# Optimization experiments

Measured on AMD Instinct MI355X. Metric: run time of the kernel, lower is better.

The kernel has to match this reference:

```python
import math
import jax, jax.numpy as jnp
import numpy as np
from jax import lax

B, N, F = 16, 1024, 35  # graphs, nodes, one-hot label width
HID = 2000

def leaky(x):
    return jnp.where(x >= 0, x, 0.01 * x)

def spp(x, levels, mode):
    # x: [C,H,W]; faithful port of spatial_pyramid_pool.spp (per-level pool,
    # flatten, zero-pad to p*p). Pool params are static Python ints.
    C, H, W = x.shape
    outs = []
    for p in range(1, levels + 1):
        kh, kw = math.ceil(H / p), math.ceil(W / p)
        ph, pw = kh * p - H, kw * p - W
        if ph * 2 > kh:
            ph = kh // 2
        if pw * 2 > kw:
            pw = kw // 2
        pad = [(0, 0), (ph, ph), (pw, pw)]
        if mode == 'max':
            r = lax.reduce_window(x, -jnp.inf, lax.max, (1, kh, kw), (1, kh, kw), pad)
        else:  # avg, count_include_pad=True (torch default)
            r = lax.reduce_window(x, 0.0, lax.add, (1, kh, kw), (1, kh, kw), pad) / (kh * kw)
        flat = r.reshape(C, -1)
        flat = jnp.pad(flat, ((0, 0), (0, p * p - flat.shape[1])))
        outs.append(flat)
    return jnp.concatenate(outs, axis=1)  # [C, sum_p p^2]

def wlc(x, masks, K):
    # Vectorized weisfeiler_lehman_conv_switch.WLC.
    # x: [N,F]; masks: [4,N,N] one-hot of edge type s in {1..4}; K: [C,T,4,F].
    # Each convo step (snapshot semantics via cal_list.clone()):
    #   x_new[i] = x[i] + sum_j [s_ij==k+1] * x[j] * K[t,k]
    def one_channel(Kc):  # Kc: [T,4,F]
        def step(xc, Kt):
            return xc + jnp.einsum('kij,jf,kf->if', masks, xc, Kt), None
        xc, _ = lax.scan(step, x, Kc)
        return xc
    return jax.vmap(one_channel)(K)  # [C,N,F]

def conv2d(x, w, b):
    y = lax.conv_general_dilated(x, w, (1, 1), 'VALID',
                                 dimension_numbers=('NCHW', 'OIHW', 'NCHW'))
    return y + b[None, :, None, None]

def setup_inputs() -> dict:
    key = jax.random.key(0)
    ks = jax.random.split(key, 16)
    lin_in = 4 * sum((i + 1) ** 2 for i in range(10)) + 5 * sum((i + 1) ** 2 for i in range(3))  # 1610
    f32 = jnp.float32
    return {
        'labelsList': jax.random.normal(ks[0], (B, N, F), f32),
        'ligand_structure': jax.random.randint(ks[1], (B, N, N), 0, 5).astype(f32),
        'K1': jax.random.normal(ks[2], (2, 2, 4, F), f32) * 0.05,
        'K2': jax.random.normal(ks[3], (2, 2, 4, F), f32) * 0.05,
        'cw1': jax.random.normal(ks[4], (2, 1, 3, 3), f32) * 0.2,
        'cb1': jnp.zeros((2,), f32),
        'cw2': jax.random.normal(ks[5], (5, 2, 3, 3), f32) * 0.1,
        'cb2': jnp.zeros((5,), f32),
        'W1': jax.random.normal(ks[6], (HID, lin_in), f32) * 0.02,
        'b1': jnp.zeros((HID,), f32),
        'W2': jax.random.normal(ks[7], (HID, HID), f32) * 0.02,
        'b2': jnp.zeros((HID,), f32),
        'W3': jax.random.normal(ks[8], (HID, HID), f32) * 0.02,
        'b3': jnp.zeros((HID,), f32),
        'W4': jax.random.normal(ks[9], (HID, HID), f32) * 0.02,
        'b4': jnp.zeros((HID,), f32),
        'W5': jax.random.normal(ks[10], (2, HID), f32) * 0.02,
        'b5': jnp.zeros((2,), f32),
    }

def reference(labelsList, ligand_structure, K1, K2, cw1, cb1, cw2, cb2,
              W1, b1, W2, b2, W3, b3, W4, b4, W5, b5):
    def per_sample(x, s):  # x: [N,F], s: [N,N]
        masks = (s[None] == jnp.arange(1.0, 5.0, dtype=s.dtype)[:, None, None]).astype(x.dtype)
        c1 = leaky(wlc(x, masks, K1))                       # [2,N,F]
        c2 = jax.vmap(lambda xc: wlc(xc, masks, K2))(c1)    # [2,2,N,F], cat order matches torch
        c2 = c2.reshape(4, N, F)
        feat = spp(leaky(c2), 10, 'max').reshape(-1)        # [1540]
        z = s[None, None]                                   # [1,1,N,N]
        z = leaky(conv2d(z, cw1, cb1))
        z = leaky(conv2d(z, cw2, cb2))                      # [1,5,N-4,N-4]
        stru = spp(z[0], 3, 'avg').reshape(-1)              # [70]
        return jnp.concatenate([feat, stru])                # [1610]

    h = jax.vmap(per_sample)(labelsList, ligand_structure)  # [B,1610]
    # fc_model (dropout = identity in eval)
    h = leaky(h @ W1.T + b1)
    h = leaky(h @ W2.T + b2)
    h = leaky(h @ W3.T + b3)
    h = leaky(h @ W4.T + b4)
    return h @ W5.T + b5                                    # [B,2]
```

## Files before the change

kernel.cpp:

```cpp
#include <hip/hip_runtime.h>
#include <stdint.h>

#define NN 1024
#define FF 35
#define LIN_IN 1610
#define NB 16

typedef short short8 __attribute__((ext_vector_type(8)));
typedef float f32x4 __attribute__((ext_vector_type(4)));
typedef float f32x2 __attribute__((ext_vector_type(2)));

__device__ __forceinline__ float leakyf(float x) { return fmaxf(x, 0.01f * x); }
__device__ __forceinline__ uint16_t to_bf16(float v) {
    return (uint16_t)((__float_as_uint(v) + 0x8000u) >> 16);
}
__device__ __forceinline__ f32x2 sp2(float s) { return (f32x2){s, s}; }
__device__ __forceinline__ f32x2 leaky2(f32x2 v) {
    f32x2 r;
    r.x = fmaxf(v.x, 0.01f * v.x);
    r.y = fmaxf(v.y, 0.01f * v.y);
    return r;
}
__device__ __forceinline__ uint32_t mapf(float x) {
    uint32_t u = __float_as_uint(x);
    return (u & 0x80000000u) ? ~u : (u | 0x80000000u);
}
__device__ __forceinline__ float unmapf(uint32_t u) {
    return (u & 0x80000000u) ? __uint_as_float(u & 0x7FFFFFFFu) : __uint_as_float(~u);
}

__global__ __launch_bounds__(256)
void codes_kernel(const float* __restrict__ s, uint8_t* __restrict__ codes, int n4) {
    int i = blockIdx.x * 256 + threadIdx.x;
    for (; i < n4; i += gridDim.x * 256) {
        float4 v = ((const float4*)s)[i];
        uchar4 c;
        c.x = (uint8_t)v.x; c.y = (uint8_t)v.y; c.z = (uint8_t)v.z; c.w = (uint8_t)v.w;
        ((uchar4*)codes)[i] = c;
    }
}

__global__ __launch_bounds__(256)
void labels_to_xt(const float* __restrict__ labels, uint16_t* __restrict__ XT0,
                  float* __restrict__ XR0)
{
    __shared__ float buf[256 * FF];
    const int s = blockIdx.x;
    const int i0 = blockIdx.y * 256;
    const float* src = labels + ((size_t)s * NN + i0) * FF;
    for (int t = threadIdx.x; t < 256 * FF; t += 256) buf[t] = src[t];
    __syncthreads();
    for (int f = 0; f < 48; ++f) {
        const int ii = threadIdx.x;
        float v = (f < FF) ? buf[ii * FF + f] : 0.f;
        size_t o = ((size_t)s * 48 + f) * 1024 + i0 + ii;
        XR0[o] = v;
        XT0[o] = to_bf16(v);
    }
}

__device__ __forceinline__ short8 expand_onehot(uint2 cd, uint32_t dupK) {
    union { uint32_t u[4]; short8 v; } r;
#pragma unroll
    for (int h = 0; h < 2; ++h) {
        uint32_t d = h ? cd.y : cd.x;
        uint32_t y = d ^ dupK;
        uint32_t m = (~(((y & 0x7F7F7F7Fu) + 0x7F7F7F7Fu) | y)) & 0x80808080u;
        uint32_t m2 = m >> 7;
        r.u[h * 2 + 0] = ((m2 & 0xFFu) | ((m2 & 0xFF00u) << 8)) * 0x3F80u;
        r.u[h * 2 + 1] = (((m2 >> 16) & 0xFFu) | ((m2 >> 8) & 0xFF0000u)) * 0x3F80u;
    }
    return r.v;
}

__device__ __forceinline__
void wlc_body(int mt, int nt, int s,
              const uint16_t* __restrict__ XT_in, const float* __restrict__ XR_in,
              uint16_t* __restrict__ XT_out, float* __restrict__ XR_out,
              const uint8_t* __restrict__ codes, const float* __restrict__ Kg,
              int t, int shift, int nch_in, int nch_out, int do_leaky)
{
    const int tid   = threadIdx.x;
    const int wid   = tid >> 6;
    const int lane  = tid & 63;
    const int chout = nt;
    const int inch  = chout >> shift;
    const int kch   = chout & 1;
    const int i0    = mt * 64 + wid * 16;

    const uint8_t* cbase = codes + ((size_t)s << 20)
        + (size_t)(i0 + (lane & 15)) * 1024 + ((lane >> 4) << 3);
    const uint16_t* bbase = XT_in + (((size_t)s * nch_in + inch) * 48 + (lane & 15)) * 1024
        + ((lane >> 4) << 3);

    f32x4 acc[4][3];
#pragma unroll
    for (int k = 0; k < 4; ++k)
#pragma unroll
        for (int nf = 0; nf < 3; ++nf) acc[k][nf] = (f32x4){0.f, 0.f, 0.f, 0.f};

#pragma unroll 2
    for (int jt = 0; jt < 16; ++jt) {
        const int j0 = jt * 64;
        const uint2 cd0 = *(const uint2*)(cbase + j0);
        const uint2 cd1 = *(const uint2*)(cbase + j0 + 32);

        short8 bfr[3][2];
#pragma unroll
        for (int nf = 0; nf < 3; ++nf)
#pragma unroll
            for (int kk = 0; kk < 2; ++kk)
                bfr[nf][kk] = *(const short8*)(bbase + (size_t)nf * 16 * 1024 + j0 + kk * 32);

#pragma unroll
        for (int k = 0; k < 4; ++k) {
            const uint32_t dupK = 0x01010101u * (k + 1);
#pragma unroll
            for (int kk = 0; kk < 2; ++kk) {
                short8 af = expand_onehot(kk ? cd1 : cd0, dupK);
#pragma unroll
                for (int nf = 0; nf < 3; ++nf)
                    acc[k][nf] = __builtin_amdgcn_mfma_f32_16x16x32_bf16(
                        af, bfr[nf][kk], acc[k][nf], 0, 0, 0);
            }
        }
    }

    float sc[4][3];
#pragma unroll
    for (int nf = 0; nf < 3; ++nf) {
        int fnl = nf * 16 + (lane & 15);
#pragma unroll
        for (int k = 0; k < 4; ++k)
            sc[k][nf] = (fnl < FF) ? Kg[((kch * 2 + t) * 4 + k) * FF + fnl] : 0.f;
    }

#pragma unroll
    for (int nf = 0; nf < 3; ++nf) {
        int fnl = nf * 16 + (lane & 15);
        int irow = i0 + ((lane >> 4) << 2);
        f32x4 rr = sc[0][nf] * acc[0][nf];
        rr += sc[1][nf] * acc[1][nf];
        rr += sc[2][nf] * acc[2][nf];
        rr += sc[3][nf] * acc[3][nf];
        size_t rb = (((size_t)s * nch_in + inch) * 48 + fnl) * 1024 + irow;
        float4 rd = *(const float4*)&XR_in[rb];
        float y0 = rr.x + rd.x, y1 = rr.y + rd.y, y2 = rr.z + rd.z, y3 = rr.w + rd.w;
        if (do_leaky) { y0 = leakyf(y0); y1 = leakyf(y1); y2 = leakyf(y2); y3 = leakyf(y3); }
        size_t ob = (((size_t)s * nch_out + chout) * 48 + fnl) * 1024 + irow;
        *(float4*)&XR_out[ob] = make_float4(y0, y1, y2, y3);
        ushort4 bv;
        bv.x = to_bf16(y0); bv.y = to_bf16(y1); bv.z = to_bf16(y2); bv.w = to_bf16(y3);
        *(ushort4*)&XT_out[ob] = bv;
    }
}

__global__ __launch_bounds__(256, 2)
void wlc_gemm(const uint16_t* __restrict__ XT_in, const float* __restrict__ XR_in,
              uint16_t* __restrict__ XT_out, float* __restrict__ XR_out,
              const uint8_t* __restrict__ codes, const float* __restrict__ Kg,
              int t, int shift, int nch_in, int nch_out, int do_leaky)
{
    wlc_body(blockIdx.x, blockIdx.y, blockIdx.z, XT_in, XR_in, XT_out, XR_out,
             codes, Kg, t, shift, nch_in, nch_out, do_leaky);
}

__device__ __forceinline__
void conv_body(int ss, int simg,
               const float* __restrict__ sM,
               const float* __restrict__ cw1, const float* __restrict__ cb1,
               const float* __restrict__ cw2, const float* __restrict__ cb2,
               float* __restrict__ h0)
{
    __shared__ float bins[30];
    const int tid  = threadIdx.x;
    const int lane = tid & 63;
    const int r0   = ss * 17;
    const int rb2  = ss / 30;
    const int rb3  = ss / 20;

    if (tid < 30) bins[tid] = 0.f;
    __syncthreads();

    const int colbase = (tid < 255) ? tid * 4 : 254 * 4;
    const float* sp = sM + (size_t)simg * (NN * NN) + colbase;

    f32x2 w1p[9], w2p[45], b1p;
#pragma unroll
    for (int i = 0; i < 9; ++i) { w1p[i].x = cw1[i]; w1p[i].y = cw1[9 + i]; }
#pragma unroll
    for (int o = 0; o < 5; ++o)
#pragma unroll
        for (int i = 0; i < 9; ++i) {
            w2p[o * 9 + i].x = cw2[(o * 2 + 0) * 9 + i];
            w2p[o * 9 + i].y = cw2[(o * 2 + 1) * 9 + i];
        }
    b1p.x = cb1[0]; b1p.y = cb1[1];
    float b2r[5];
#pragma unroll
    for (int i = 0; i < 5; ++i) b2r[i] = cb2[i];

    float sw[3][8];
    f32x2 z1w[3][6];
    float acc[5][4];
#pragma unroll
    for (int o = 0; o < 5; ++o)
#pragma unroll
        for (int j = 0; j < 4; ++j) acc[o][j] = 0.f;

#define LOADROW(slot, rabs) do { \
    float4 v0 = *(const float4*)(sp + (size_t)(rabs) * NN); \
    float4 v1 = *(const float4*)(sp + (size_t)(rabs) * NN + 4); \
    sw[slot][0]=v0.x; sw[slot][1]=v0.y; sw[slot][2]=v0.z; sw[slot][3]=v0.w; \
    sw[slot][4]=v1.x; sw[slot][5]=v1.y; sw[slot][6]=v1.z; sw[slot][7]=v1.w; } while(0)

#define Z1ROW(P) do { \
    _Pragma("unroll") for (int jj = 0; jj < 6; ++jj) { \
        f32x2 a = b1p; \
        _Pragma("unroll") for (int dc = 0; dc < 3; ++dc) { \
            a += sp2(sw[((P)+2)%3][jj+dc]) * w1p[0+dc]; \
            a += sp2(sw[(P)%3    ][jj+dc]) * w1p[3+dc]; \
            a += sp2(sw[((P)+1)%3][jj+dc]) * w1p[6+dc]; } \
        z1w[((P)+2)%3][jj] = leaky2(a); } } while(0)

#define Z2ROW(P) do { \
    _Pragma("unroll") for (int o = 0; o < 5; ++o) { \
      _Pragma("unroll") for (int j = 0; j < 4; ++j) { \
        f32x2 a = (f32x2){b2r[o], 0.f}; \
        _Pragma("unroll") for (int dc = 0; dc < 3; ++dc) { \
            a += z1w[(P)%3    ][j+dc] * w2p[o*9+0+dc]; \
            a += z1w[((P)+1)%3][j+dc] * w2p[o*9+3+dc]; \
            a += z1w[((P)+2)%3][j+dc] * w2p[o*9+6+dc]; } \
        float sres = a.x + a.y; \
        acc[o][j] += fmaxf(sres, 0.01f * sres); } } } while(0)

    LOADROW(0, r0 + 0);
    LOADROW(1, r0 + 1);
    LOADROW(2, r0 + 2);
    Z1ROW(1);
    LOADROW(0, r0 + 3);
    Z1ROW(2);

#pragma unroll 1
    for (int rr = 0; rr < 15; rr += 3) {
        LOADROW(1, r0 + rr + 4); Z1ROW(0); Z2ROW(0);
        LOADROW(2, r0 + rr + 5); Z1ROW(1); Z2ROW(1);
        LOADROW(0, r0 + rr + 6); Z1ROW(2); Z2ROW(2);
    }
    LOADROW(1, r0 + 19); Z1ROW(0); Z2ROW(0);
    LOADROW(2, r0 + 20); Z1ROW(1); Z2ROW(1);

#undef LOADROW
#undef Z1ROW
#undef Z2ROW

    if (tid == 255) {
#pragma unroll
        for (int o = 0; o < 5; ++o)
#pragma unroll
            for (int j = 0; j < 4; ++j) acc[o][j] = 0.f;
    }

    int cb2c[4], cb3c[4];
#pragma unroll
    for (int j = 0; j < 4; ++j) {
        int col = colbase + j;
        int a2 = col / 510; if (a2 > 1) a2 = 1;
        int a3 = col / 340; if (a3 > 2) a3 = 2;
        cb2c[j] = a2; cb3c[j] = a3;
    }

#pragma unroll
    for (int o = 0; o < 5; ++o) {
        float t1 = acc[o][0] + acc[o][1] + acc[o][2] + acc[o][3];
        float pa = 0.f, pb = 0.f, q0 = 0.f, q1 = 0.f, q2 = 0.f;
#pragma unroll
        for (int j = 0; j < 4; ++j) {
            float v = acc[o][j];
            if (cb2c[j] == 0) pa += v; else pb += v;
            if (cb3c[j] == 0) q0 += v; else if (cb3c[j] == 1) q1 += v; else q2 += v;
        }
#pragma unroll
        for (int d = 32; d >= 1; d >>= 1) {
            t1 += __shfl_xor(t1, d, 64);
            pa += __shfl_xor(pa, d, 64);
            pb += __shfl_xor(pb, d, 64);
            q0 += __shfl_xor(q0, d, 64);
            q1 += __shfl_xor(q1, d, 64);
            q2 += __shfl_xor(q2, d, 64);
        }
        if (lane == 0) {
            atomicAdd(&bins[o * 6 + 0], t1);
            atomicAdd(&bins[o * 6 + 1], pa);
            atomicAdd(&bins[o * 6 + 2], pb);
            atomicAdd(&bins[o * 6 + 3], q0);
            atomicAdd(&bins[o * 6 + 4], q1);
            atomicAdd(&bins[o * 6 + 5], q2);
        }
    }
    __syncthreads();
    if (tid < 30) {
        int o = tid / 6, b = tid % 6;
        int off; float scale;
        if (b == 0)      { off = 0;                         scale = 1.f / (1020.f * 1020.f); }
        else if (b <= 2) { off = 1 + rb2 * 2 + (b - 1);     scale = 1.f / (510.f * 510.f); }
        else             { off = 5 + rb3 * 3 + (b - 3);     scale = 1.f / (340.f * 340.f); }
        atomicAdd(h0 + (size_t)simg * LIN_IN + 1540 + o * 14 + off, bins[tid] * scale);
    }
}

__global__ __launch_bounds__(256, 2)
void fused_wlc_conv(int convBlocks, int imgBase,
                    const float* __restrict__ sM,
                    const float* __restrict__ cw1, const float* __restrict__ cb1,
                    const float* __restrict__ cw2, const float* __restrict__ cb2,
                    float* __restrict__ h0,
                    const uint16_t* __restrict__ XT_in, const float* __restrict__ XR_in,
                    uint16_t* __restrict__ XT_out, float* __restrict__ XR_out,
                    const uint8_t* __restrict__ codes, const float* __restrict__ Kg,
                    int t, int shift, int nch_in, int nch_out, int do_leaky)
{
    const int bid = blockIdx.x;
    if (bid < convBlocks) {
        conv_body(bid % 60, imgBase + bid / 60, sM, cw1, cb1, cw2, cb2, h0);
    } else {
        const int b = bid - convBlocks;
        wlc_body(b & 15, (b >> 4) & 3, b >> 6, XT_in, XR_in, XT_out, XR_out,
                 codes, Kg, t, shift, nch_in, nch_out, do_leaky);
    }
}

__global__ __launch_bounds__(256)
void spp_scatter_kernel(const float* __restrict__ xr4, uint32_t* __restrict__ scratch)
{
    constexpr int KH[10] = {1024, 512, 342, 256, 205, 171, 147, 128, 114, 103};
    constexpr int PH[10] = {0, 0, 2, 0, 1, 2, 5, 0, 2, 6};
    constexpr int KW[10] = {35, 18, 12, 9, 7, 6, 5, 5, 4, 4};
    constexpr int PW[10] = {0, 1, 1, 1, 0, 1, 0, 2, 1, 2};
    constexpr int OW[10] = {1, 2, 3, 4, 5, 6, 7, 7, 9, 9};
    constexpr int BASE[10] = {0, 1, 5, 14, 30, 55, 91, 140, 204, 285};

    __shared__ uint32_t cells[385];
    const int b  = blockIdx.x;
    const int rq = b & 3;
    const int c  = (b >> 2) & 3;
    const int s  = b >> 4;
    const int r  = rq * 256 + threadIdx.x;

    for (int i = threadIdx.x; i < 385; i += 256) cells[i] = 0u;
    __syncthreads();

    const float* bp = xr4 + ((size_t)s * 4 + c) * (48 * 1024) + r;

    int addr[10];
#pragma unroll
    for (int pi = 0; pi < 10; ++pi)
        addr[pi] = BASE[pi] + ((r + PH[pi]) / KH[pi]) * OW[pi];

    float acc[10];
#pragma unroll
    for (int pi = 0; pi < 10; ++pi) acc[pi] = -3.402823466e38f;

#pragma unroll
    for (int f = 0; f < FF; ++f) {
        const float v = bp[(size_t)f * 1024];
#pragma unroll
        for (int pi = 0; pi < 10; ++pi) {
            const int cbin = (f + PW[pi]) / KW[pi];
            const int cbn  = (f + 1 < FF) ? ((f + 1 + PW[pi]) / KW[pi]) : -1;
            if (cbin < OW[pi]) {
                acc[pi] = fmaxf(acc[pi], v);
                if (cbn != cbin) {
                    atomicMax(&cells[addr[pi] + cbin], mapf(acc[pi]));
                    acc[pi] = -3.402823466e38f;
                }
            }
        }
    }

    __syncthreads();
    for (int i = threadIdx.x; i < 385; i += 256) {
        uint32_t u = cells[i];
        if (u) atomicMax(&scratch[((size_t)s * 4 + c) * 385 + i], u);
    }
}

__global__ __launch_bounds__(256)
void spp_unmap_kernel(const uint32_t* __restrict__ scratch, float* __restrict__ h0)
{
    constexpr int OHW[10] = {1, 4, 9, 16, 25, 36, 49, 56, 81, 90};
    const int idx = blockIdx.x * 256 + threadIdx.x;
    if (idx >= NB * 4 * 385) return;
    const int s = idx / (4 * 385);
    int rem = idx - s * (4 * 385);
    const int c = rem / 385;
    const int cell = rem - c * 385;

    int p1 = 1, base = 0;
    while (p1 < 10 && cell >= base + p1 * p1) { base += p1 * p1; ++p1; }
    const int ci = cell - base;
    if (ci >= OHW[p1 - 1]) return;

    h0[(size_t)s * LIN_IN + c * 385 + cell] = unmapf(scratch[idx]);
}

template<int VEC>
__global__ __launch_bounds__(256)
void fc_kernel(const float* __restrict__ in, const float* __restrict__ W,
               const float* __restrict__ bias, float* __restrict__ out,
               int K, int Nout, int do_leaky)
{
    const int o = (blockIdx.x * 256 + threadIdx.x) >> 6;
    const int lane = threadIdx.x & 63;
    if (o >= Nout) return;
    const float* wrow = W + (size_t)o * K;
    float acc[16];
#pragma unroll
    for (int b = 0; b < 16; ++b) acc[b] = 0.f;

    const int step = 64 * VEC;
    const int kmain = (K / step) * step;
#pragma unroll 2
    for (int k0 = 0; k0 < kmain; k0 += step) {
        const int kk = k0 + lane * VEC;
        if (VEC == 4) {
            float4 w = *(const float4*)(wrow + kk);
#pragma unroll
            for (int b = 0; b < 16; ++b) {
                float4 h = *(const float4*)(in + (size_t)b * K + kk);
                acc[b] += w.x * h.x + w.y * h.y + w.z * h.z + w.w * h.w;
            }
        } else {
            float2 w = *(const float2*)(wrow + kk);
#pragma unroll
            for (int b = 0; b < 16; ++b) {
                float2 h = *(const float2*)(in + (size_t)b * K + kk);
                acc[b] += w.x * h.x + w.y * h.y;
            }
        }
    }
    {
        const int kk = kmain + lane * VEC;
        if (kk < K) {
            if (VEC == 4) {
                float4 w = *(const float4*)(wrow + kk);
#pragma unroll
                for (int b = 0; b < 16; ++b) {
                    float4 h = *(const float4*)(in + (size_t)b * K + kk);
                    acc[b] += w.x * h.x + w.y * h.y + w.z * h.z + w.w * h.w;
                }
            } else {
                float2 w = *(const float2*)(wrow + kk);
#pragma unroll
                for (int b = 0; b < 16; ++b) {
                    float2 h = *(const float2*)(in + (size_t)b * K + kk);
                    acc[b] += w.x * h.x + w.y * h.y;
                }
            }
        }
    }

    float res = 0.f;
#pragma unroll
    for (int b = 0; b < 16; ++b) {
        float v = acc[b];
#pragma unroll
        for (int od = 32; od >= 1; od >>= 1) v += __shfl_xor(v, od, 64);
        if (lane == b) res = v;
    }
    if (lane < 16) {
        const float y = res + bias[o];
        out[(size_t)lane * Nout + o] = do_leaky ? leakyf(y) : y;
    }
}

extern "C" void kernel_launch(void* const* d_in, const int* in_sizes, int n_in,
                              void* d_out, int out_size, void* d_ws, size_t ws_size,
                              hipStream_t stream)
{
    const float* labels = (const float*)d_in[0];
    const float* sM     = (const float*)d_in[1];
    const float* K1     = (const float*)d_in[2];
    const float* K2     = (const float*)d_in[3];
    const float* cw1    = (const float*)d_in[4];
    const float* cb1    = (const float*)d_in[5];
    const float* cw2    = (const float*)d_in[6];
    const float* cb2    = (const float*)d_in[7];
    const float* W1     = (const float*)d_in[8];
    const float* b1     = (const float*)d_in[9];
    const float* W2     = (const float*)d_in[10];
    const float* b2     = (const float*)d_in[11];
    const float* W3     = (const float*)d_in[12];
    const float* b3     = (const float*)d_in[13];
    const float* W4     = (const float*)d_in[14];
    const float* b4     = (const float*)d_in[15];
    const float* W5     = (const float*)d_in[16];
    const float* b5     = (const float*)d_in[17];

    char* ws = (char*)d_ws;
    uint8_t* codes = (uint8_t*)ws;  ws += (size_t)16 << 20;
    char* ping = ws;                ws += 18874368;
    char* pong = ws;                ws += 18874368;
    float* h0  = (float*)ws;        ws += 103168;
    float* hA  = (float*)ws;        ws += 128000;
    float* hB  = (float*)ws;        ws += 128000;
    uint32_t* sppbuf = (uint32_t*)ws; ws += (size_t)NB * 4 * 385 * 4;

    uint16_t* XTp = (uint16_t*)ping; float* XRp = (float*)(ping + 6291456);
    uint16_t* XTq = (uint16_t*)pong; float* XRq = (float*)(pong + 6291456);

    hipMemsetAsync(h0, 0, (size_t)NB * LIN_IN * 4, stream);
    hipMemsetAsync(sppbuf, 0, (size_t)NB * 4 * 385 * 4, stream);

    codes_kernel<<<2048, 256, 0, stream>>>(sM, codes, 16 * 1024 * 1024 / 4);
    labels_to_xt<<<dim3(16, 4), 256, 0, stream>>>(labels, XTq, XRq);

    wlc_gemm<<<dim3(16, 2, 16), 256, 0, stream>>>(XTq, XRq, XTp, XRp, codes, K1, 0, 1, 1, 2, 0);
    wlc_gemm<<<dim3(16, 2, 16), 256, 0, stream>>>(XTp, XRp, XTq, XRq, codes, K1, 1, 0, 2, 2, 1);

    fused_wlc_conv<<<480 + 1024, 256, 0, stream>>>(
        480, 0, sM, cw1, cb1, cw2, cb2, h0,
        XTq, XRq, XTp, XRp, codes, K2, 0, 1, 2, 4, 0);
    fused_wlc_conv<<<480 + 1024, 256, 0, stream>>>(
        480, 8, sM, cw1, cb1, cw2, cb2, h0,
        XTp, XRp, XTq, XRq, codes, K2, 1, 0, 4, 4, 1);

    spp_scatter_kernel<<<256, 256, 0, stream>>>(XRq, sppbuf);
    spp_unmap_kernel<<<(NB * 4 * 385 + 255) / 256, 256, 0, stream>>>(sppbuf, h0);

    fc_kernel<2><<<500, 256, 0, stream>>>(h0, W1, b1, hA, LIN_IN, 2000, 1);
    fc_kernel<4><<<500, 256, 0, stream>>>(hA, W2, b2, hB, 2000, 2000, 1);
    fc_kernel<4><<<500, 256, 0, stream>>>(hB, W3, b3, hA, 2000, 2000, 1);
    fc_kernel<4><<<500, 256, 0, stream>>>(hA, W4, b4, hB, 2000, 2000, 1);
    fc_kernel<4><<<1,   256, 0, stream>>>(hB, W5, b5, (float*)d_out, 2000, 2, 0);
}
```

Before: 334.6 us.

## Split conv work into half-width blocks and spread across all four WLC launches

Each conv block now covers half of the columns and splits its 17-row strip into two 9/8-row halves across thread halves, which doubles the conv block count to 1920. These blocks are then spread evenly over all four WLC step launches, including the two K1 steps that used to run as plain wlc_gemm. The aim is to overlap conv work with the lighter K1 GEMMs and shorten the critical path of the two K2 launches. In exchange, the overlapping halo rows and columns are loaded redundantly and an extra column-masking step is needed.

```diff
diff --git a/kernel.cpp b/kernel.cpp
--- a/kernel.cpp
+++ b/kernel.cpp
@@ -155,34 +155,29 @@
     }
 }
 
-__global__ __launch_bounds__(256, 2)
-void wlc_gemm(const uint16_t* __restrict__ XT_in, const float* __restrict__ XR_in,
-              uint16_t* __restrict__ XT_out, float* __restrict__ XR_out,
-              const uint8_t* __restrict__ codes, const float* __restrict__ Kg,
-              int t, int shift, int nch_in, int nch_out, int do_leaky)
-{
-    wlc_body(blockIdx.x, blockIdx.y, blockIdx.z, XT_in, XR_in, XT_out, XR_out,
-             codes, Kg, t, shift, nch_in, nch_out, do_leaky);
-}
-
 __device__ __forceinline__
-void conv_body(int ss, int simg,
+void conv_body(int ss, int hh, int simg,
                const float* __restrict__ sM,
                const float* __restrict__ cw1, const float* __restrict__ cb1,
                const float* __restrict__ cw2, const float* __restrict__ cb2,
                float* __restrict__ h0)
 {
     __shared__ float bins[30];
-    const int tid  = threadIdx.x;
-    const int lane = tid & 63;
-    const int r0   = ss * 17;
-    const int rb2  = ss / 30;
-    const int rb3  = ss / 20;
+    const int tid   = threadIdx.x;
+    const int lane  = tid & 63;
+    const int t128  = tid & 127;
+    const int rh    = tid >> 7;
+    const int r0    = ss * 17;
+    const int rbase = r0 + rh * 9;
+    const int rb2   = ss / 30;
+    const int rb3   = ss / 20;
 
     if (tid < 30) bins[tid] = 0.f;
     __syncthreads();
 
-    const int colbase = (tid < 255) ? tid * 4 : 254 * 4;
+    const int rawbase = hh * 510 + t128 * 4;
+    const int collim  = hh * 510 + 510;
+    const int colbase = (rawbase > 1016) ? 1016 : rawbase;
     const float* sp = sM + (size_t)simg * (NN * NN) + colbase;
 
     f32x2 w1p[9], w2p[45], b1p;
@@ -234,31 +229,43 @@
         float sres = a.x + a.y; \
         acc[o][j] += fmaxf(sres, 0.01f * sres); } } } while(0)
 
-    LOADROW(0, r0 + 0);
-    LOADROW(1, r0 + 1);
-    LOADROW(2, r0 + 2);
+#define STEPX(P, t) do { \
+    LOADROW(((P)+1)%3, rbase + (t) + 4); \
+    Z1ROW(P); \
+    Z2ROW(P); } while(0)
+
+    LOADROW(0, rbase + 0);
+    LOADROW(1, rbase + 1);
+    LOADROW(2, rbase + 2);
     Z1ROW(1);
-    LOADROW(0, r0 + 3);
+    LOADROW(0, rbase + 3);
     Z1ROW(2);
 
+    if (rh == 0) {
 #pragma unroll 1
-    for (int rr = 0; rr < 15; rr += 3) {
-        LOADROW(1, r0 + rr + 4); Z1ROW(0); Z2ROW(0);
-        LOADROW(2, r0 + rr + 5); Z1ROW(1); Z2ROW(1);
-        LOADROW(0, r0 + rr + 6); Z1ROW(2); Z2ROW(2);
-    }
-    LOADROW(1, r0 + 19); Z1ROW(0); Z2ROW(0);
-    LOADROW(2, r0 + 20); Z1ROW(1); Z2ROW(1);
+        for (int t = 0; t < 9; t += 3) {
+            STEPX(0, t); STEPX(1, t + 1); STEPX(2, t + 2);
+        }
+    } else {
+#pragma unroll 1
+        for (int t = 0; t < 6; t += 3) {
+            STEPX(0, t); STEPX(1, t + 1); STEPX(2, t + 2);
+        }
+        STEPX(0, 6); STEPX(1, 7);
+    }
 
 #undef LOADROW
 #undef Z1ROW
 #undef Z2ROW
-
-    if (tid == 255) {
-#pragma unroll
-        for (int o = 0; o < 5; ++o)
-#pragma unroll
-            for (int j = 0; j < 4; ++j) acc[o][j] = 0.f;
+#undef STEPX
+
+#pragma unroll
+    for (int j = 0; j < 4; ++j) {
+        const int c = colbase + j;
+        if (c < rawbase || c >= collim) {
+#pragma unroll
+            for (int o = 0; o < 5; ++o) acc[o][j] = 0.f;
+        }
     }
 
     int cb2c[4], cb3c[4];
@@ -310,7 +317,7 @@
 }
 
 __global__ __launch_bounds__(256, 2)
-void fused_wlc_conv(int convBlocks, int imgBase,
+void fused_wlc_conv(int convBlocks, int convBase, int nsh,
                     const float* __restrict__ sM,
                     const float* __restrict__ cw1, const float* __restrict__ cb1,
                     const float* __restrict__ cw2, const float* __restrict__ cb2,
@@ -322,10 +329,14 @@
 {
     const int bid = blockIdx.x;
     if (bid < convBlocks) {
-        conv_body(bid % 60, imgBase + bid / 60, sM, cw1, cb1, cw2, cb2, h0);
+        const int g = convBase + bid;
+        conv_body(g % 60, (g / 60) & 1, g / 120, sM, cw1, cb1, cw2, cb2, h0);
     } else {
-        const int b = bid - convBlocks;
-        wlc_body(b & 15, (b >> 4) & 3, b >> 6, XT_in, XR_in, XT_out, XR_out,
+        const int w = bid - convBlocks;
+        const int mt = w & 15;
+        const int nt = (w >> 4) & ((1 << nsh) - 1);
+        const int s  = w >> (4 + nsh);
+        wlc_body(mt, nt, s, XT_in, XR_in, XT_out, XR_out,
                  codes, Kg, t, shift, nch_in, nch_out, do_leaky);
     }
 }
@@ -515,14 +526,17 @@
     codes_kernel<<<2048, 256, 0, stream>>>(sM, codes, 16 * 1024 * 1024 / 4);
     labels_to_xt<<<dim3(16, 4), 256, 0, stream>>>(labels, XTq, XRq);
 
-    wlc_gemm<<<dim3(16, 2, 16), 256, 0, stream>>>(XTq, XRq, XTp, XRp, codes, K1, 0, 1, 1, 2, 0);
-    wlc_gemm<<<dim3(16, 2, 16), 256, 0, stream>>>(XTp, XRp, XTq, XRq, codes, K1, 1, 0, 2, 2, 1);
-
+    fused_wlc_conv<<<480 + 512, 256, 0, stream>>>(
+        480, 0, 1, sM, cw1, cb1, cw2, cb2, h0,
+        XTq, XRq, XTp, XRp, codes, K1, 0, 1, 1, 2, 0);
+    fused_wlc_conv<<<480 + 512, 256, 0, stream>>>(
+        480, 480, 1, sM, cw1, cb1, cw2, cb2, h0,
+        XTp, XRp, XTq, XRq, codes, K1, 1, 0, 2, 2, 1);
     fused_wlc_conv<<<480 + 1024, 256, 0, stream>>>(
-        480, 0, sM, cw1, cb1, cw2, cb2, h0,
+        480, 960, 2, sM, cw1, cb1, cw2, cb2, h0,
         XTq, XRq, XTp, XRp, codes, K2, 0, 1, 2, 4, 0);
     fused_wlc_conv<<<480 + 1024, 256, 0, stream>>>(
-        480, 8, sM, cw1, cb1, cw2, cb2, h0,
+        480, 1440, 2, sM, cw1, cb1, cw2, cb2, h0,
         XTp, XRp, XTq, XRq, codes, K2, 1, 0, 4, 4, 1);
 
     spp_scatter_kernel<<<256, 256, 0, stream>>>(XRq, sppbuf);
```

New measurement: 352.6 us. 1.05x slower.
